# Kernel tuning notes

Hardware: AMD Instinct MI355X
Metric: run time of the kernel (lower is better)

The kernel has to match this reference:

```python
import jax, jax.numpy as jnp
import numpy as np

NQ = 4  # n_qubits
C64 = jnp.complex64
INV_SQRT2 = np.float32(1.0 / np.sqrt(2.0))
H_GATE = jnp.array([[1.0, 1.0], [1.0, -1.0]], dtype=C64) * INV_SQRT2


def _apply_1q(state, U, q):
    # state: (B, 2,2,2,2) complex; U: (2,2) shared or (B,2,2) per-batch
    s = jnp.moveaxis(state, q + 1, -1)
    if U.ndim == 2:
        s = jnp.einsum('b...i,ji->b...j', s, U)
    else:
        s = jnp.einsum('b...i,bji->b...j', s, U)
    return jnp.moveaxis(s, -1, q + 1)


def _apply_cnot(state, c, t):
    s = jnp.moveaxis(state, (c + 1, t + 1), (-2, -1))
    s = jnp.stack([s[..., 0, :], s[..., 1, ::-1]], axis=-2)  # flip target when control=1
    return jnp.moveaxis(s, (-2, -1), (c + 1, t + 1))


def _ry(theta):
    co = jnp.cos(theta * 0.5).astype(C64)
    si = jnp.sin(theta * 0.5).astype(C64)
    return jnp.stack([jnp.stack([co, -si], -1), jnp.stack([si, co], -1)], -2)


def _rz(theta):
    e = jnp.exp(-0.5j * theta).astype(C64)
    z = jnp.zeros_like(e)
    return jnp.stack([jnp.stack([e, z], -1), jnp.stack([z, jnp.conj(e)], -1)], -2)


def _rx(theta):
    co = jnp.cos(theta * 0.5).astype(C64)
    si = (-1j * jnp.sin(theta * 0.5)).astype(C64)
    return jnp.stack([jnp.stack([co, si], -1), jnp.stack([si, co], -1)], -2)


def _vqc(y, w):
    # y: (B, NQ) float angles-to-encode; w: (n_qlayers, 3, NQ)
    B = y.shape[0]
    state = jnp.zeros((B, 2 ** NQ), C64).at[:, 0].set(1.0).reshape((B,) + (2,) * NQ)
    ry_ang = jnp.arctan(y)
    rz_ang = jnp.arctan(y * y)
    # encoding: H, RY(arctan y), RZ(arctan y^2) on each wire
    for q in range(NQ):
        state = _apply_1q(state, H_GATE, q)
        state = _apply_1q(state, _ry(ry_ang[:, q]), q)
        state = _apply_1q(state, _rz(rz_ang[:, q]), q)
    # ansatz layers: CNOT ring (n_esteps=1), then RX/RY/RZ with weights
    for l in range(w.shape[0]):
        for q in range(NQ):
            state = _apply_cnot(state, q, (q + 1) % NQ)
        for q in range(NQ):
            state = _apply_1q(state, _rx(w[l, 0, q]), q)
            state = _apply_1q(state, _ry(w[l, 1, q]), q)
            state = _apply_1q(state, _rz(w[l, 2, q]), q)
    probs = state.real ** 2 + state.imag ** 2  # (B,2,2,2,2)
    outs = []
    for q in range(NQ):
        p = jnp.moveaxis(probs, q + 1, 1).reshape(B, 2, -1).sum(-1)
        outs.append(p[:, 0] - p[:, 1])  # <Z_q>
    return jnp.stack(outs, -1).astype(y.dtype)


def _qlstm(x, W_in, b_in, W_out, b_out, w_f, w_i, w_u, w_o):
    B = x.shape[0]
    Hdim = W_out.shape[1]
    h0 = jnp.zeros((B, Hdim), x.dtype)
    c0 = jnp.zeros((B, Hdim), x.dtype)

    def step(carry, x_t):
        h, c = carry
        y = jnp.concatenate([h, x_t], axis=1) @ W_in + b_in  # (B, NQ)
        f = jax.nn.sigmoid(_vqc(y, w_f) @ W_out + b_out)
        i = jax.nn.sigmoid(_vqc(y, w_i) @ W_out + b_out)
        g = jnp.tanh(_vqc(y, w_u) @ W_out + b_out)
        o = jax.nn.sigmoid(_vqc(y, w_o) @ W_out + b_out)
        c = f * c + i * g
        h = o * jnp.tanh(c)
        return (h, c), h

    (hT, cT), outs = jax.lax.scan(step, (h0, c0), jnp.swapaxes(x, 0, 1))
    return jnp.swapaxes(outs, 0, 1), hT, cT


def setup_inputs() -> dict:
    key = jax.random.key(0)
    ks = jax.random.split(key, 9)
    B, S, D, Hdim = 512, 256, 64, 128
    x = jax.random.normal(ks[0], (B, S, D), jnp.float32)
    W_in = jax.random.normal(ks[1], (Hdim + D, NQ), jnp.float32) * 0.1
    b_in = jax.random.normal(ks[2], (NQ,), jnp.float32) * 0.1
    W_out = jax.random.normal(ks[3], (NQ, Hdim), jnp.float32) * 0.1
    b_out = jax.random.normal(ks[4], (Hdim,), jnp.float32) * 0.1
    two_pi = np.float32(2.0 * np.pi)
    w_f = jax.random.uniform(ks[5], (1, 3, NQ), jnp.float32, 0.0, two_pi)
    w_i = jax.random.uniform(ks[6], (1, 3, NQ), jnp.float32, 0.0, two_pi)
    w_u = jax.random.uniform(ks[7], (1, 3, NQ), jnp.float32, 0.0, two_pi)
    w_o = jax.random.uniform(ks[8], (1, 3, NQ), jnp.float32, 0.0, two_pi)
    return {'x': x, 'W_in': W_in, 'b_in': b_in, 'W_out': W_out, 'b_out': b_out,
            'w_f': w_f, 'w_i': w_i, 'w_u': w_u, 'w_o': w_o}


def reference(x, W_in, b_in, W_out, b_out, w_f, w_i, w_u, w_o):
    return _qlstm(x, W_in, b_in, W_out, b_out, w_f, w_i, w_u, w_o)
```

## Files before the change

### kernel.cpp

```cpp
#include <hip/hip_runtime.h>
#include <math.h>

#define B_TOT 512
#define S_LEN 256
#define D_IN  64
#define HDIM  128

typedef float v2f __attribute__((ext_vector_type(2)));

__device__ __forceinline__ float rcp_f(float x) { return __builtin_amdgcn_rcpf(x); }
__device__ __forceinline__ float rsq_f(float x) { return __builtin_amdgcn_rsqf(x); }

__device__ __forceinline__ v2f fma2(v2f a, v2f b, v2f c) { return __builtin_elementwise_fma(a, b, c); }
__device__ __forceinline__ v2f splat2(float s) { v2f r = {s, s}; return r; }

__device__ __forceinline__ v2f sig2(v2f s) {
    v2f e = { __expf(-s.x), __expf(-s.y) };
    v2f ONE = {1.f, 1.f};
    v2f d = e + ONE;
    v2f r = { rcp_f(d.x), rcp_f(d.y) };
    return r;
}
__device__ __forceinline__ v2f tanh2(v2f s) {
    v2f t = s + s;
    v2f e = { __expf(t.x), __expf(t.y) };
    v2f ONE = {1.f, 1.f};
    v2f d = e + ONE;
    v2f r = { rcp_f(d.x), rcp_f(d.y) };
    v2f NTWO = {-2.f, -2.f};
    return fma2(r, NTWO, ONE);
}

template<int CTRL>
__device__ __forceinline__ float dpp_add(float v) {
    int t = __builtin_amdgcn_update_dpp(0, __float_as_int(v), CTRL, 0xF, 0xF, true);
    return v + __int_as_float(t);
}

__device__ __forceinline__ float allsum64(float v, int idx32) {
    v = dpp_add<0xB1>(v);
    v = dpp_add<0x4E>(v);
    v = dpp_add<0x141>(v);
    v = dpp_add<0x140>(v);
    int s = __builtin_amdgcn_ds_swizzle(__float_as_int(v), 0x401F);
    v += __int_as_float(s);
    int t = __builtin_amdgcn_ds_bpermute(idx32, __float_as_int(v));
    v += __int_as_float(t);
    return v;
}

__global__ void __launch_bounds__(64, 1) xproj_kernel(
    const float* __restrict__ x,
    const float* __restrict__ Win,
    const float* __restrict__ bin,
    float4* __restrict__ yx)
{
    const int l  = threadIdx.x;
    const int b  = blockIdx.x >> 4;
    const int t0 = (blockIdx.x & 15) << 4;
    const int idx32 = (l ^ 32) << 2;

    const float4 wx = reinterpret_cast<const float4*>(Win)[128 + l];
    const v2f wxa = {wx.x, wx.y}, wxb = {wx.z, wx.w};
    const float4 bn = *reinterpret_cast<const float4*>(bin);

    const float* xp = x + ((size_t)b * S_LEN + t0) * D_IN + l;
    float4* yp = yx + (size_t)b * S_LEN + t0;

#pragma unroll 4
    for (int tt = 0; tt < 16; ++tt) {
        float xv = xp[(size_t)tt * D_IN];
        v2f p01 = splat2(xv) * wxa;
        v2f p23 = splat2(xv) * wxb;
        float y0 = allsum64(p01.x, idx32);
        float y1 = allsum64(p01.y, idx32);
        float y2 = allsum64(p23.x, idx32);
        float y3 = allsum64(p23.y, idx32);
        if (l == 0)
            yp[tt] = make_float4(y0 + bn.x, y1 + bn.y, y2 + bn.z, y3 + bn.w);
    }
}

template<bool PRE>
__global__ void __launch_bounds__(64, 1) qlstm_kernel(
    const float* __restrict__ x,
    const float* __restrict__ Win,
    const float* __restrict__ bin,
    const float* __restrict__ Wout,
    const float* __restrict__ bout,
    const float* __restrict__ wf,
    const float* __restrict__ wi,
    const float* __restrict__ wu,
    const float* __restrict__ wo,
    float* __restrict__ out,
    const float4* __restrict__ yx)
{
    const int l = threadIdx.x;
    const int b = blockIdx.x;
    const int idx32 = (l ^ 32) << 2;

    const float4* W4 = reinterpret_cast<const float4*>(Win);
    const float4 r0 = W4[2 * l];
    const float4 r1 = W4[2 * l + 1];
    const v2f wh0a = {r0.x, r0.y}, wh0b = {r0.z, r0.w};
    const v2f wh1a = {r1.x, r1.y}, wh1b = {r1.z, r1.w};

    v2f wxa = {0.f, 0.f}, wxb = {0.f, 0.f}, bna = {0.f, 0.f}, bnb = {0.f, 0.f};
    if (!PRE) {
        const float4 rx = W4[128 + l];
        wxa.x = rx.x; wxa.y = rx.y; wxb.x = rx.z; wxb.y = rx.w;
        const float4 bn = *reinterpret_cast<const float4*>(bin);
        bna.x = bn.x * 0.015625f; bna.y = bn.y * 0.015625f;
        bnb.x = bn.z * 0.015625f; bnb.y = bn.w * 0.015625f;
    }

    v2f Wo[4];
#pragma unroll
    for (int q = 0; q < 4; ++q) {
        Wo[q].x = Wout[q * HDIM + 2 * l];
        Wo[q].y = Wout[q * HDIM + 2 * l + 1];
    }
    const v2f bo = {bout[2 * l], bout[2 * l + 1]};

    v2f UX[4][2], UY[4][2], UZ[4][2];
    {
        const float* wg[4] = {wf, wi, wu, wo};
#pragma unroll
        for (int g = 0; g < 4; ++g) {
#pragma unroll
            for (int p = 0; p < 2; ++p) {
#pragma unroll
                for (int e = 0; e < 2; ++e) {
                    int q = 2 * p + e;
                    float a  = wg[g][q];
                    float be = wg[g][4 + q];
                    float sa = sinf(a),  ca = cosf(a);
                    float sb = sinf(be), cb = cosf(be);
                    UX[g][p][e] = -sb;
                    UY[g][p][e] = cb * sa;
                    UZ[g][p][e] = cb * ca;
                }
            }
        }
    }

    v2f h = {0.f, 0.f}, c = {0.f, 0.f};
    const v2f ONE = {1.f, 1.f};

    float* ob = out + (size_t)b * (S_LEN * HDIM) + 2 * l;

    const float4* yxp = PRE ? (yx + (size_t)b * S_LEN) : nullptr;
    const float*  xb  = PRE ? nullptr : (x + (size_t)b * (S_LEN * D_IN) + l);
    float4 ya, yb;
    float  xa, xv_b;
    if (PRE) { ya = yxp[0]; yb = yxp[1]; }
    else     { xa = xb[0];  xv_b = xb[D_IN]; }

    for (int t = 0; t < S_LEN; ++t) {
        v2f p01, p23;
        float4 ycur;
        if (PRE) {
            ycur = ya; ya = yb;
            int tn = t + 2; if (tn > S_LEN - 1) tn = S_LEN - 1;
            yb = yxp[tn];
            p01 = fma2(splat2(h.y), wh1a, splat2(h.x) * wh0a);
            p23 = fma2(splat2(h.y), wh1b, splat2(h.x) * wh0b);
        } else {
            float xv = xa; xa = xv_b;
            int tn = t + 2; if (tn > S_LEN - 1) tn = S_LEN - 1;
            xv_b = xb[(size_t)tn * D_IN];
            p01 = fma2(splat2(h.y), wh1a, fma2(splat2(h.x), wh0a, fma2(splat2(xv), wxa, bna)));
            p23 = fma2(splat2(h.y), wh1b, fma2(splat2(h.x), wh0b, fma2(splat2(xv), wxb, bnb)));
        }

        float y0 = allsum64(p01.x, idx32);
        float y1 = allsum64(p01.y, idx32);
        float y2 = allsum64(p23.x, idx32);
        float y3 = allsum64(p23.y, idx32);

        v2f yA = {y0, y1}, yB = {y2, y3};
        if (PRE) {
            v2f xc0 = {ycur.x, ycur.y}, xc1 = {ycur.z, ycur.w};
            yA = yA + xc0;
            yB = yB + xc1;
        }

        v2f qA = yA * yA,  qB = yB * yB;
        v2f aA = fma2(yA, yA, ONE), aB = fma2(yB, yB, ONE);
        v2f bA = fma2(qA, qA, ONE), bB = fma2(qB, qB, ONE);
        v2f r1A = { rsq_f(aA.x), rsq_f(aA.y) };
        v2f r1B = { rsq_f(aB.x), rsq_f(aB.y) };
        v2f r2A = { rsq_f(bA.x), rsq_f(bA.y) };
        v2f r2B = { rsq_f(bB.x), rsq_f(bB.y) };
        v2f nxA = r1A * r2A, nxB = r1B * r2B;
        v2f nyA = qA * nxA,  nyB = qB * nxB;
        v2f nzA = -(yA * r1A), nzB = -(yB * r1B);
        float nx0 = nxA.x, nx1 = nxA.y, nx2 = nxB.x, nx3 = nxB.y;
        float ny0 = nyA.x, ny1 = nyA.y, ny2 = nyB.x, ny3 = nyB.y;
        float nz0 = nzA.x, nz1 = nzA.y, nz2 = nzB.x, nz3 = nzB.y;

        float nz01 = nz0 * nz1;
        float nz23 = nz2 * nz3;
        v2f TXa, TXb, TYa, TYb, TZa, TZb;
        TXa.x = nx0 * nx1;  TXa.y = nx1 * nx2;
        TXb.x = nx2 * nx3;  TXb.y = TXa.x * nx3;
        TZa.x = nz1 * nz23; TZa.y = nz01;
        TZb.x = nz01 * nz2; TZb.y = nz01 * nz23;
        TYa.x = (nx0 * ny1) * nz23;  TYa.y = (nz0 * ny1) * nx2;
        TYb.x = (nz01 * ny2) * nx3;  TYb.y = -(ny0 * ny1) * (nz2 * ny3);

        v2f pre[4];
#pragma unroll
        for (int g = 0; g < 4; ++g) {
            v2f za = fma2(UX[g][0], TXa, fma2(UY[g][0], TYa, UZ[g][0] * TZa));
            v2f zb = fma2(UX[g][1], TXb, fma2(UY[g][1], TYb, UZ[g][1] * TZb));
            v2f s = fma2(splat2(za.x), Wo[0], bo);
            s = fma2(splat2(za.y), Wo[1], s);
            s = fma2(splat2(zb.x), Wo[2], s);
            s = fma2(splat2(zb.y), Wo[3], s);
            pre[g] = s;
        }

        v2f fg = sig2(pre[0]);
        v2f ig = sig2(pre[1]);
        v2f gg = tanh2(pre[2]);
        v2f og = sig2(pre[3]);
        c = fma2(fg, c, ig * gg);
        h = og * tanh2(c);

        *reinterpret_cast<v2f*>(ob + (size_t)t * HDIM) = h;
    }

    float* hT = out + (size_t)B_TOT * S_LEN * HDIM;
    float* cT = hT + (size_t)B_TOT * HDIM;
    *reinterpret_cast<v2f*>(hT + (size_t)b * HDIM + 2 * l) = h;
    *reinterpret_cast<v2f*>(cT + (size_t)b * HDIM + 2 * l) = c;
}

extern "C" void kernel_launch(void* const* d_in, const int* in_sizes, int n_in,
                              void* d_out, int out_size, void* d_ws, size_t ws_size,
                              hipStream_t stream) {
    const size_t yx_bytes = (size_t)B_TOT * S_LEN * 4 * sizeof(float);
    if (d_ws != nullptr && ws_size >= yx_bytes) {
        float4* yx = (float4*)d_ws;
        xproj_kernel<<<dim3(B_TOT * 16), dim3(64), 0, stream>>>(
            (const float*)d_in[0], (const float*)d_in[1], (const float*)d_in[2], yx);
        qlstm_kernel<true><<<dim3(B_TOT), dim3(64), 0, stream>>>(
            (const float*)d_in[0], (const float*)d_in[1], (const float*)d_in[2],
            (const float*)d_in[3], (const float*)d_in[4],
            (const float*)d_in[5], (const float*)d_in[6],
            (const float*)d_in[7], (const float*)d_in[8],
            (float*)d_out, yx);
    } else {
        qlstm_kernel<false><<<dim3(B_TOT), dim3(64), 0, stream>>>(
            (const float*)d_in[0], (const float*)d_in[1], (const float*)d_in[2],
            (const float*)d_in[3], (const float*)d_in[4],
            (const float*)d_in[5], (const float*)d_in[6],
            (const float*)d_in[7], (const float*)d_in[8],
            (float*)d_out, nullptr);
    }
}
```

Baseline: 239.6 us.

## Use inline-asm DPP row_bcast reductions and stage projected inputs in LDS

Replaces the per-value wave reduction (DPP plus ds_swizzle plus bpermute) with a single inline-asm block that reduces four values together using DPP quad_perm, mirror and row_bcast adds, then one bpermute from lane 63 to broadcast. The aim is to interleave the four independent reductions and remove the swizzle from the serial recurrence's critical path. The precomputed input projections are also staged into shared memory once per block, so the per-timestep global load becomes an LDS read. The risks are that the asm volatile block limits compiler scheduling and relies on hand-placed nops for DPP hazards. Also, yxl[t+2] is read past the 256 written entries at the last steps; those values are never used.

```diff
diff --git a/kernel.cpp b/kernel.cpp
--- a/kernel.cpp
+++ b/kernel.cpp
@@ -31,22 +31,43 @@
     return fma2(r, NTWO, ONE);
 }
 
-template<int CTRL>
-__device__ __forceinline__ float dpp_add(float v) {
-    int t = __builtin_amdgcn_update_dpp(0, __float_as_int(v), CTRL, 0xF, 0xF, true);
-    return v + __int_as_float(t);
-}
-
-__device__ __forceinline__ float allsum64(float v, int idx32) {
-    v = dpp_add<0xB1>(v);
-    v = dpp_add<0x4E>(v);
-    v = dpp_add<0x141>(v);
-    v = dpp_add<0x140>(v);
-    int s = __builtin_amdgcn_ds_swizzle(__float_as_int(v), 0x401F);
-    v += __int_as_float(s);
-    int t = __builtin_amdgcn_ds_bpermute(idx32, __float_as_int(v));
-    v += __int_as_float(t);
-    return v;
+__device__ __forceinline__ void reduce4(float p0, float p1, float p2, float p3,
+                                        float& y0, float& y1, float& y2, float& y3,
+                                        int bidx) {
+    asm volatile(
+        "s_nop 1\n\t"
+        "v_add_f32 %0, %0, %0 quad_perm:[1,0,3,2] row_mask:0xf bank_mask:0xf\n\t"
+        "v_add_f32 %1, %1, %1 quad_perm:[1,0,3,2] row_mask:0xf bank_mask:0xf\n\t"
+        "v_add_f32 %2, %2, %2 quad_perm:[1,0,3,2] row_mask:0xf bank_mask:0xf\n\t"
+        "v_add_f32 %3, %3, %3 quad_perm:[1,0,3,2] row_mask:0xf bank_mask:0xf\n\t"
+        "v_add_f32 %0, %0, %0 quad_perm:[2,3,0,1] row_mask:0xf bank_mask:0xf\n\t"
+        "v_add_f32 %1, %1, %1 quad_perm:[2,3,0,1] row_mask:0xf bank_mask:0xf\n\t"
+        "v_add_f32 %2, %2, %2 quad_perm:[2,3,0,1] row_mask:0xf bank_mask:0xf\n\t"
+        "v_add_f32 %3, %3, %3 quad_perm:[2,3,0,1] row_mask:0xf bank_mask:0xf\n\t"
+        "v_add_f32 %0, %0, %0 row_half_mirror row_mask:0xf bank_mask:0xf\n\t"
+        "v_add_f32 %1, %1, %1 row_half_mirror row_mask:0xf bank_mask:0xf\n\t"
+        "v_add_f32 %2, %2, %2 row_half_mirror row_mask:0xf bank_mask:0xf\n\t"
+        "v_add_f32 %3, %3, %3 row_half_mirror row_mask:0xf bank_mask:0xf\n\t"
+        "v_add_f32 %0, %0, %0 row_mirror row_mask:0xf bank_mask:0xf\n\t"
+        "v_add_f32 %1, %1, %1 row_mirror row_mask:0xf bank_mask:0xf\n\t"
+        "v_add_f32 %2, %2, %2 row_mirror row_mask:0xf bank_mask:0xf\n\t"
+        "v_add_f32 %3, %3, %3 row_mirror row_mask:0xf bank_mask:0xf\n\t"
+        "v_add_f32 %0, %0, %0 row_bcast:15 row_mask:0xf bank_mask:0xf bound_ctrl:0\n\t"
+        "v_add_f32 %1, %1, %1 row_bcast:15 row_mask:0xf bank_mask:0xf bound_ctrl:0\n\t"
+        "v_add_f32 %2, %2, %2 row_bcast:15 row_mask:0xf bank_mask:0xf bound_ctrl:0\n\t"
+        "v_add_f32 %3, %3, %3 row_bcast:15 row_mask:0xf bank_mask:0xf bound_ctrl:0\n\t"
+        "v_add_f32 %0, %0, %0 row_bcast:31 row_mask:0xf bank_mask:0xf bound_ctrl:0\n\t"
+        "v_add_f32 %1, %1, %1 row_bcast:31 row_mask:0xf bank_mask:0xf bound_ctrl:0\n\t"
+        "v_add_f32 %2, %2, %2 row_bcast:31 row_mask:0xf bank_mask:0xf bound_ctrl:0\n\t"
+        "v_add_f32 %3, %3, %3 row_bcast:31 row_mask:0xf bank_mask:0xf bound_ctrl:0\n\t"
+        "ds_bpermute_b32 %4, %8, %0\n\t"
+        "ds_bpermute_b32 %5, %8, %1\n\t"
+        "ds_bpermute_b32 %6, %8, %2\n\t"
+        "ds_bpermute_b32 %7, %8, %3\n\t"
+        "s_waitcnt lgkmcnt(0)"
+        : "+v"(p0), "+v"(p1), "+v"(p2), "+v"(p3),
+          "=&v"(y0), "=&v"(y1), "=&v"(y2), "=&v"(y3)
+        : "v"(bidx));
 }
 
 __global__ void __launch_bounds__(64, 1) xproj_kernel(
@@ -58,10 +79,9 @@
     const int l  = threadIdx.x;
     const int b  = blockIdx.x >> 4;
     const int t0 = (blockIdx.x & 15) << 4;
-    const int idx32 = (l ^ 32) << 2;
+    const int bidx = 252;
 
     const float4 wx = reinterpret_cast<const float4*>(Win)[128 + l];
-    const v2f wxa = {wx.x, wx.y}, wxb = {wx.z, wx.w};
     const float4 bn = *reinterpret_cast<const float4*>(bin);
 
     const float* xp = x + ((size_t)b * S_LEN + t0) * D_IN + l;
@@ -70,12 +90,8 @@
 #pragma unroll 4
     for (int tt = 0; tt < 16; ++tt) {
         float xv = xp[(size_t)tt * D_IN];
-        v2f p01 = splat2(xv) * wxa;
-        v2f p23 = splat2(xv) * wxb;
-        float y0 = allsum64(p01.x, idx32);
-        float y1 = allsum64(p01.y, idx32);
-        float y2 = allsum64(p23.x, idx32);
-        float y3 = allsum64(p23.y, idx32);
+        float y0, y1, y2, y3;
+        reduce4(xv * wx.x, xv * wx.y, xv * wx.z, xv * wx.w, y0, y1, y2, y3, bidx);
         if (l == 0)
             yp[tt] = make_float4(y0 + bn.x, y1 + bn.y, y2 + bn.z, y3 + bn.w);
     }
@@ -97,7 +113,9 @@
 {
     const int l = threadIdx.x;
     const int b = blockIdx.x;
-    const int idx32 = (l ^ 32) << 2;
+    const int bidx = 252;
+
+    __shared__ float4 yxl[S_LEN + 2];
 
     const float4* W4 = reinterpret_cast<const float4*>(Win);
     const float4 r0 = W4[2 * l];
@@ -112,6 +130,11 @@
         const float4 bn = *reinterpret_cast<const float4*>(bin);
         bna.x = bn.x * 0.015625f; bna.y = bn.y * 0.015625f;
         bnb.x = bn.z * 0.015625f; bnb.y = bn.w * 0.015625f;
+    } else {
+        const float4* yxg = yx + (size_t)b * S_LEN;
+#pragma unroll
+        for (int k = 0; k < 4; ++k)
+            yxl[(k << 6) + l] = yxg[(k << 6) + l];
     }
 
     v2f Wo[4];
@@ -149,20 +172,15 @@
 
     float* ob = out + (size_t)b * (S_LEN * HDIM) + 2 * l;
 
-    const float4* yxp = PRE ? (yx + (size_t)b * S_LEN) : nullptr;
-    const float*  xb  = PRE ? nullptr : (x + (size_t)b * (S_LEN * D_IN) + l);
-    float4 ya, yb;
-    float  xa, xv_b;
-    if (PRE) { ya = yxp[0]; yb = yxp[1]; }
-    else     { xa = xb[0];  xv_b = xb[D_IN]; }
+    float4 ycur, yn;
+    const float* xb = PRE ? nullptr : (x + (size_t)b * (S_LEN * D_IN) + l);
+    float xa = 0.f, xv_b = 0.f;
+    if (PRE) { ycur = yxl[0]; yn = yxl[1]; }
+    else     { xa = xb[0];    xv_b = xb[D_IN]; }
 
     for (int t = 0; t < S_LEN; ++t) {
         v2f p01, p23;
-        float4 ycur;
         if (PRE) {
-            ycur = ya; ya = yb;
-            int tn = t + 2; if (tn > S_LEN - 1) tn = S_LEN - 1;
-            yb = yxp[tn];
             p01 = fma2(splat2(h.y), wh1a, splat2(h.x) * wh0a);
             p23 = fma2(splat2(h.y), wh1b, splat2(h.x) * wh0b);
         } else {
@@ -173,10 +191,8 @@
             p23 = fma2(splat2(h.y), wh1b, fma2(splat2(h.x), wh0b, fma2(splat2(xv), wxb, bnb)));
         }
 
-        float y0 = allsum64(p01.x, idx32);
-        float y1 = allsum64(p01.y, idx32);
-        float y2 = allsum64(p23.x, idx32);
-        float y3 = allsum64(p23.y, idx32);
+        float y0, y1, y2, y3;
+        reduce4(p01.x, p01.y, p23.x, p23.y, y0, y1, y2, y3, bidx);
 
         v2f yA = {y0, y1}, yB = {y2, y3};
         if (PRE) {
@@ -184,6 +200,9 @@
             yA = yA + xc0;
             yB = yB + xc1;
         }
+
+        float4 yread2;
+        if (PRE) yread2 = yxl[t + 2];
 
         v2f qA = yA * yA,  qB = yB * yB;
         v2f aA = fma2(yA, yA, ONE), aB = fma2(yB, yB, ONE);
@@ -227,6 +246,8 @@
         v2f og = sig2(pre[3]);
         c = fma2(fg, c, ig * gg);
         h = og * tanh2(c);
+
+        if (PRE) { ycur = yn; yn = yread2; }
 
         *reinterpret_cast<v2f*>(ob + (size_t)t * HDIM) = h;
     }
```

Result: faster. 223.6 us (-6.6%).
